# Performance work log

Measured on AMD Instinct MI355X. Metric: run time of the kernel, lower is better.

Reference implementation:

```python
import jax, jax.numpy as jnp
import numpy as np

B = 131072   # batched ODE states
D = 32       # state dim (net1 in/out)
H1 = 50      # net1 hidden
Q = 528      # tril(outer(y,y)) feature count = D*(D+1)//2
H2 = 700     # net2 hidden

# static lower-triangular index pairs for the quadratic feature expansion
_ROWS, _COLS = np.tril_indices(D)
_ROWS = jnp.asarray(_ROWS)
_COLS = jnp.asarray(_COLS)


def setup_inputs() -> dict:
    key = jax.random.key(0)
    ks = jax.random.split(key, 6)
    y = jax.random.normal(ks[0], (B, D), dtype=jnp.float32)
    t = jnp.zeros((1,), dtype=jnp.float32)  # unused by the dynamics
    # weights init: normal(0, 0.1), biases zero (as in the torch module)
    W1a = 0.1 * jax.random.normal(ks[1], (D, H1), dtype=jnp.float32)
    b1a = jnp.zeros((H1,), dtype=jnp.float32)
    W1b = 0.1 * jax.random.normal(ks[2], (H1, D), dtype=jnp.float32)
    b1b = jnp.zeros((D,), dtype=jnp.float32)
    W2a = 0.1 * jax.random.normal(ks[3], (Q, H2), dtype=jnp.float32)
    b2a = jnp.zeros((H2,), dtype=jnp.float32)
    W2b = 0.1 * jax.random.normal(ks[4], (H2, D), dtype=jnp.float32)
    b2b = jnp.zeros((D,), dtype=jnp.float32)
    return dict(t=t, y=y, W1a=W1a, b1a=b1a, W1b=W1b, b1b=b1b,
                W2a=W2a, b2a=b2a, W2b=W2b, b2b=b2b)


def reference(t, y, W1a, b1a, W1b, b1b, W2a, b2a, W2b, b2b):
    # quadratic_y: lower triangle of outer(y, y), vectorized over batch
    quad = y[:, _ROWS] * y[:, _COLS]               # [B, 528]
    out1 = jnp.tanh(y @ W1a + b1a) @ W1b + b1b     # [B, 32]
    out2 = jnp.tanh(quad @ W2a + b2a) @ W2b + b2b  # [B, 32]
    return out1 + out2
```

## Files before the change

kernel.cpp:

```cpp
#include <hip/hip_runtime.h>
#include <hip/hip_bf16.h>

#define B_TOT 131072
#define D     32
#define H1    50
#define QF    528
#define H2    700
#define MROWS 32
#define QSTR  584
#define KITER 18

typedef __attribute__((ext_vector_type(8))) short  short8x;
typedef __attribute__((ext_vector_type(4))) float  floatx4;

static __device__ __forceinline__ unsigned short f2bf(float f) {
    __hip_bfloat16 h = __float2bfloat16(f);
    return __builtin_bit_cast(unsigned short, h);
}
static __device__ __forceinline__ float bf2f(unsigned short u) {
    unsigned int x = (unsigned int)u << 16;
    return __builtin_bit_cast(float, x);
}
static __device__ __forceinline__ float tanh_fast(float x) {
    float e = __builtin_amdgcn_exp2f(x * 2.885390082f);
    return 1.f - 2.f * __builtin_amdgcn_rcpf(e + 1.f);
}

__global__ void prep_kernel(const float* __restrict__ W2a, const float* __restrict__ b2a,
                            const float* __restrict__ W2b,
                            const float* __restrict__ W1a, const float* __restrict__ b1a,
                            const float* __restrict__ W1b, const float* __restrict__ b1b,
                            const float* __restrict__ b2b,
                            unsigned short* __restrict__ W2aT,
                            unsigned short* __restrict__ W2bT) {
    int idx = blockIdx.x * 256 + threadIdx.x;
    const int N1 = KITER * 48 * 512;
    const int N2 = 16 * 4 * 512;
    if (idx < N1) {
        int k   = idx / (48 * 512);
        int rem = idx - k * (48 * 512);
        int p   = rem >> 9;
        int q   = rem & 511;
        int ln  = q >> 3, j = q & 7;
        int kk  = k * 32 + ((ln >> 4) << 3) + j;
        int c   = (p << 4) + (ln & 15);
        float v = 0.f;
        if (c < H2) {
            if (kk < QF)       v = W2a[kk * H2 + c];
            else if (kk == QF) v = b2a[c];
        } else if (c < H2 + H1) {
            int cc = c - H2;
            if (kk == QF)                        v = b1a[cc];
            else if (kk > QF && kk < QF + 1 + D) v = W1a[(kk - QF - 1) * H1 + cc];
        } else if (c == H2 + H1) {
            if (kk == QF) v = 1.0f;
        }
        W2aT[idx] = f2bf(v);
    } else if (idx < N1 + N2) {
        int i2 = idx - N1;
        int q  = i2 & 511;
        int ln = q >> 3, j = q & 7;
        int w  = i2 >> 11;
        int ks = (i2 >> 10) & 1;
        int of = (i2 >> 9) & 1;
        int kl = (ks << 5) + ((ln >> 4) << 3) + j;
        int kg = w * 48 + kl;
        int c  = (of << 4) + (ln & 15);
        float v = 0.f;
        if (kl < 48) {
            if (kg < H2)            v = W2b[kg * D + c];
            else if (kg < H2 + H1)  v = W1b[(kg - H2) * D + c];
            else if (kg == H2 + H1) v = (b1b[c] + b2b[c]) / tanh_fast(1.0f);
        }
        W2bT[i2] = f2bf(v);
    }
}

__global__ __launch_bounds__(1024, 8)
__attribute__((amdgpu_waves_per_eu(8, 8)))
void fused_kernel(
    const float* __restrict__ y,
    const unsigned short* __restrict__ W2aT, const unsigned short* __restrict__ W2bT,
    float* __restrict__ out) {

    __shared__ unsigned short quadls[MROWS][QSTR];
    __shared__ float          yls[MROWS][36];
    __shared__ unsigned short hst[16][16][68];

    const int tid  = threadIdx.x;
    const int lane = tid & 63;
    const int w    = tid >> 6;
    const int wu   = __builtin_amdgcn_readfirstlane(w);
    const int l15  = lane & 15;
    const int lg   = lane >> 4;
    const int row0 = blockIdx.x * MROWS;

    yls[tid >> 5][tid & 31] = y[row0 * D + tid];
    {
        int rr = lane >> 2, cc0 = 48 + (lane & 3) * 4;
        *reinterpret_cast<unsigned long long*>(&hst[w][rr][cc0]) = 0ULL;
    }
    __syncthreads();

    {
        int r = tid >> 5, i = tid & 31;
        int base = (i * (i + 1)) >> 1;
        float yi = yls[r][i];
        for (int j4 = 0; j4 <= i; j4 += 4) {
            floatx4 yv = *reinterpret_cast<const floatx4*>(&yls[r][j4]);
            #pragma unroll
            for (int jj = 0; jj < 4; ++jj) {
                int j = j4 + jj;
                if (j <= i) quadls[r][base + j] = f2bf(yi * yv[jj]);
            }
        }
        quadls[r][529 + i] = f2bf(yi);
        if (i == 0)  quadls[r][528] = (unsigned short)0x3F80;
        if (i < 15)  quadls[r][561 + i] = 0;
    }
    __syncthreads();

    floatx4 hacc00 = {0,0,0,0}, hacc01 = {0,0,0,0}, hacc02 = {0,0,0,0};
    floatx4 hacc10 = {0,0,0,0}, hacc11 = {0,0,0,0}, hacc12 = {0,0,0,0};
    {
        const unsigned short* bp = W2aT + wu * 3 * 512 + lane * 8;
        #pragma unroll 1
        for (int k = 0; k < KITER; ++k) {
            short8x a0 = *reinterpret_cast<const short8x*>(&quadls[l15][k * 32 + lg * 8]);
            short8x a1 = *reinterpret_cast<const short8x*>(&quadls[16 + l15][k * 32 + lg * 8]);
            short8x b0 = *reinterpret_cast<const short8x*>(bp);
            short8x b1 = *reinterpret_cast<const short8x*>(bp + 512);
            short8x b2 = *reinterpret_cast<const short8x*>(bp + 1024);
            hacc00 = __builtin_amdgcn_mfma_f32_16x16x32_bf16(a0, b0, hacc00, 0, 0, 0);
            hacc01 = __builtin_amdgcn_mfma_f32_16x16x32_bf16(a0, b1, hacc01, 0, 0, 0);
            hacc02 = __builtin_amdgcn_mfma_f32_16x16x32_bf16(a0, b2, hacc02, 0, 0, 0);
            hacc10 = __builtin_amdgcn_mfma_f32_16x16x32_bf16(a1, b0, hacc10, 0, 0, 0);
            hacc11 = __builtin_amdgcn_mfma_f32_16x16x32_bf16(a1, b1, hacc11, 0, 0, 0);
            hacc12 = __builtin_amdgcn_mfma_f32_16x16x32_bf16(a1, b2, hacc12, 0, 0, 0);
            bp += 48 * 512;
        }
    }
    __syncthreads();

    unsigned short* stage = &quadls[0][0];
    {
        const unsigned short* wb = W2bT + wu * 4 * 512 + lane * 8;
        #pragma unroll
        for (int m = 0; m < 2; ++m) {
            const floatx4 h0 = m ? hacc10 : hacc00;
            const floatx4 h1 = m ? hacc11 : hacc01;
            const floatx4 h2 = m ? hacc12 : hacc02;
            #pragma unroll
            for (int r = 0; r < 4; ++r) {
                hst[w][lg * 4 + r][l15]      = f2bf(tanh_fast(h0[r]));
                hst[w][lg * 4 + r][16 + l15] = f2bf(tanh_fast(h1[r]));
                hst[w][lg * 4 + r][32 + l15] = f2bf(tanh_fast(h2[r]));
            }
            short8x aa0 = *reinterpret_cast<const short8x*>(&hst[w][l15][lg * 8]);
            short8x aa1 = *reinterpret_cast<const short8x*>(&hst[w][l15][32 + lg * 8]);
            floatx4 o20 = {0,0,0,0}, o21 = {0,0,0,0};
            {
                short8x bw00 = *reinterpret_cast<const short8x*>(wb);
                short8x bw01 = *reinterpret_cast<const short8x*>(wb + 512);
                o20 = __builtin_amdgcn_mfma_f32_16x16x32_bf16(aa0, bw00, o20, 0, 0, 0);
                o21 = __builtin_amdgcn_mfma_f32_16x16x32_bf16(aa0, bw01, o21, 0, 0, 0);
            }
            {
                short8x bw10 = *reinterpret_cast<const short8x*>(wb + 1024);
                short8x bw11 = *reinterpret_cast<const short8x*>(wb + 1536);
                o20 = __builtin_amdgcn_mfma_f32_16x16x32_bf16(aa1, bw10, o20, 0, 0, 0);
                o21 = __builtin_amdgcn_mfma_f32_16x16x32_bf16(aa1, bw11, o21, 0, 0, 0);
            }
            #pragma unroll
            for (int r = 0; r < 4; ++r) {
                int row = m * 16 + lg * 4 + r;
                unsigned int pk = ((unsigned int)f2bf(o21[r]) << 16) | (unsigned int)f2bf(o20[r]);
                *reinterpret_cast<unsigned int*>(&stage[wu * 1024 + row * 32 + l15 * 2]) = pk;
            }
        }
    }
    __syncthreads();

    {
        int c  = tid & 31;
        int fr = (tid & ~31) + ((c & 15) << 1) + (c >> 4);
        float s0 = 0.f, s1 = 0.f;
        #pragma unroll
        for (int p = 0; p < 16; p += 2) {
            s0 += bf2f(stage[p * 1024 + fr]);
            s1 += bf2f(stage[(p + 1) * 1024 + fr]);
        }
        out[row0 * D + tid] = s0 + s1;
    }
}

extern "C" void kernel_launch(void* const* d_in, const int* in_sizes, int n_in,
                              void* d_out, int out_size, void* d_ws, size_t ws_size,
                              hipStream_t stream) {
    const float* y   = (const float*)d_in[1];
    const float* W1a = (const float*)d_in[2];
    const float* b1a = (const float*)d_in[3];
    const float* W1b = (const float*)d_in[4];
    const float* b1b = (const float*)d_in[5];
    const float* W2a = (const float*)d_in[6];
    const float* b2a = (const float*)d_in[7];
    const float* W2b = (const float*)d_in[8];
    const float* b2b = (const float*)d_in[9];

    unsigned short* W2aT = (unsigned short*)d_ws;
    unsigned short* W2bT = (unsigned short*)((char*)d_ws + 884736);

    const int prep_tasks = KITER * 48 * 512 + 16 * 4 * 512;
    prep_kernel<<<(prep_tasks + 255) / 256, 256, 0, stream>>>(
        W2a, b2a, W2b, W1a, b1a, W1b, b1b, b2b, W2aT, W2bT);
    fused_kernel<<<B_TOT / MROWS, 1024, 0, stream>>>(y, W2aT, W2bT, (float*)d_out);
}
```

Before: 164.4 us.

## Loop multiple row tiles per block and store quad features in MFMA fragment layout

Each block now processes 8 consecutive 32-row tiles in a loop, cutting the grid size by 8x. The quadratic features are scattered into LDS in the exact per-lane MFMA A-fragment order, so the GEMM loop reads contiguous 16-byte chunks per lane instead of strided rows. This aims to cut launch/tail overhead and LDS bank conflicts, at the cost of no overlap between tiles and scattered 2-byte LDS writes during feature construction.

```diff
diff --git a/kernel.cpp b/kernel.cpp
--- a/kernel.cpp
+++ b/kernel.cpp
@@ -7,8 +7,8 @@
 #define QF    528
 #define H2    700
 #define MROWS 32
-#define QSTR  584
 #define KITER 18
+#define TILES 8
 
 typedef __attribute__((ext_vector_type(8))) short  short8x;
 typedef __attribute__((ext_vector_type(4))) float  floatx4;
@@ -83,7 +83,7 @@
     const unsigned short* __restrict__ W2aT, const unsigned short* __restrict__ W2bT,
     float* __restrict__ out) {
 
-    __shared__ unsigned short quadls[MROWS][QSTR];
+    __shared__ unsigned short quadA[KITER][2][512];
     __shared__ float          yls[MROWS][36];
     __shared__ unsigned short hst[16][16][68];
 
@@ -93,104 +93,122 @@
     const int wu   = __builtin_amdgcn_readfirstlane(w);
     const int l15  = lane & 15;
     const int lg   = lane >> 4;
-    const int row0 = blockIdx.x * MROWS;
-
-    yls[tid >> 5][tid & 31] = y[row0 * D + tid];
+    unsigned short* stage = &quadA[0][0][0];
+
     {
         int rr = lane >> 2, cc0 = 48 + (lane & 3) * 4;
         *reinterpret_cast<unsigned long long*>(&hst[w][rr][cc0]) = 0ULL;
     }
-    __syncthreads();
-
-    {
-        int r = tid >> 5, i = tid & 31;
-        int base = (i * (i + 1)) >> 1;
-        float yi = yls[r][i];
-        for (int j4 = 0; j4 <= i; j4 += 4) {
-            floatx4 yv = *reinterpret_cast<const floatx4*>(&yls[r][j4]);
+
+    for (int t = 0; t < TILES; ++t) {
+        const int row0 = (blockIdx.x * TILES + t) * MROWS;
+
+        yls[tid >> 5][tid & 31] = y[row0 * D + tid];
+        __syncthreads();
+
+        {
+            int r = tid >> 5, i = tid & 31;
+            int rbase = ((r >> 4) << 9) + ((r & 15) << 3);
+            int base  = (i * (i + 1)) >> 1;
+            float yi  = yls[r][i];
+            for (int j4 = 0; j4 <= i; j4 += 4) {
+                floatx4 yv = *reinterpret_cast<const floatx4*>(&yls[r][j4]);
+                #pragma unroll
+                for (int jj = 0; jj < 4; ++jj) {
+                    int j = j4 + jj;
+                    if (j <= i) {
+                        int kk = base + j;
+                        stage[rbase + ((kk >> 5) << 10) + ((kk & 24) << 4) + (kk & 7)]
+                            = f2bf(yi * yv[jj]);
+                    }
+                }
+            }
+            {
+                int kk = 529 + i;
+                stage[rbase + ((kk >> 5) << 10) + ((kk & 24) << 4) + (kk & 7)] = f2bf(yi);
+            }
+            if (i == 0)
+                stage[rbase + ((528 >> 5) << 10) + ((528 & 24) << 4)] = (unsigned short)0x3F80;
+            if (i < 15) {
+                int kk = 561 + i;
+                stage[rbase + ((kk >> 5) << 10) + ((kk & 24) << 4) + (kk & 7)] = 0;
+            }
+        }
+        __syncthreads();
+
+        floatx4 hacc00 = {0,0,0,0}, hacc01 = {0,0,0,0}, hacc02 = {0,0,0,0};
+        floatx4 hacc10 = {0,0,0,0}, hacc11 = {0,0,0,0}, hacc12 = {0,0,0,0};
+        {
+            const unsigned short* bp = W2aT + wu * 3 * 512 + lane * 8;
+            const unsigned short* ap = &quadA[0][0][lane * 8];
+            #pragma unroll 1
+            for (int k = 0; k < KITER; ++k) {
+                short8x a0 = *reinterpret_cast<const short8x*>(ap);
+                short8x a1 = *reinterpret_cast<const short8x*>(ap + 512);
+                short8x b0 = *reinterpret_cast<const short8x*>(bp);
+                short8x b1 = *reinterpret_cast<const short8x*>(bp + 512);
+                short8x b2 = *reinterpret_cast<const short8x*>(bp + 1024);
+                hacc00 = __builtin_amdgcn_mfma_f32_16x16x32_bf16(a0, b0, hacc00, 0, 0, 0);
+                hacc01 = __builtin_amdgcn_mfma_f32_16x16x32_bf16(a0, b1, hacc01, 0, 0, 0);
+                hacc02 = __builtin_amdgcn_mfma_f32_16x16x32_bf16(a0, b2, hacc02, 0, 0, 0);
+                hacc10 = __builtin_amdgcn_mfma_f32_16x16x32_bf16(a1, b0, hacc10, 0, 0, 0);
+                hacc11 = __builtin_amdgcn_mfma_f32_16x16x32_bf16(a1, b1, hacc11, 0, 0, 0);
+                hacc12 = __builtin_amdgcn_mfma_f32_16x16x32_bf16(a1, b2, hacc12, 0, 0, 0);
+                ap += 1024;
+                bp += 48 * 512;
+            }
+        }
+        __syncthreads();
+
+        {
+            const unsigned short* wb = W2bT + wu * 4 * 512 + lane * 8;
             #pragma unroll
-            for (int jj = 0; jj < 4; ++jj) {
-                int j = j4 + jj;
-                if (j <= i) quadls[r][base + j] = f2bf(yi * yv[jj]);
-            }
-        }
-        quadls[r][529 + i] = f2bf(yi);
-        if (i == 0)  quadls[r][528] = (unsigned short)0x3F80;
-        if (i < 15)  quadls[r][561 + i] = 0;
-    }
-    __syncthreads();
-
-    floatx4 hacc00 = {0,0,0,0}, hacc01 = {0,0,0,0}, hacc02 = {0,0,0,0};
-    floatx4 hacc10 = {0,0,0,0}, hacc11 = {0,0,0,0}, hacc12 = {0,0,0,0};
-    {
-        const unsigned short* bp = W2aT + wu * 3 * 512 + lane * 8;
-        #pragma unroll 1
-        for (int k = 0; k < KITER; ++k) {
-            short8x a0 = *reinterpret_cast<const short8x*>(&quadls[l15][k * 32 + lg * 8]);
-            short8x a1 = *reinterpret_cast<const short8x*>(&quadls[16 + l15][k * 32 + lg * 8]);
-            short8x b0 = *reinterpret_cast<const short8x*>(bp);
-            short8x b1 = *reinterpret_cast<const short8x*>(bp + 512);
-            short8x b2 = *reinterpret_cast<const short8x*>(bp + 1024);
-            hacc00 = __builtin_amdgcn_mfma_f32_16x16x32_bf16(a0, b0, hacc00, 0, 0, 0);
-            hacc01 = __builtin_amdgcn_mfma_f32_16x16x32_bf16(a0, b1, hacc01, 0, 0, 0);
-            hacc02 = __builtin_amdgcn_mfma_f32_16x16x32_bf16(a0, b2, hacc02, 0, 0, 0);
-            hacc10 = __builtin_amdgcn_mfma_f32_16x16x32_bf16(a1, b0, hacc10, 0, 0, 0);
-            hacc11 = __builtin_amdgcn_mfma_f32_16x16x32_bf16(a1, b1, hacc11, 0, 0, 0);
-            hacc12 = __builtin_amdgcn_mfma_f32_16x16x32_bf16(a1, b2, hacc12, 0, 0, 0);
-            bp += 48 * 512;
-        }
-    }
-    __syncthreads();
-
-    unsigned short* stage = &quadls[0][0];
-    {
-        const unsigned short* wb = W2bT + wu * 4 * 512 + lane * 8;
-        #pragma unroll
-        for (int m = 0; m < 2; ++m) {
-            const floatx4 h0 = m ? hacc10 : hacc00;
-            const floatx4 h1 = m ? hacc11 : hacc01;
-            const floatx4 h2 = m ? hacc12 : hacc02;
+            for (int m = 0; m < 2; ++m) {
+                const floatx4 h0 = m ? hacc10 : hacc00;
+                const floatx4 h1 = m ? hacc11 : hacc01;
+                const floatx4 h2 = m ? hacc12 : hacc02;
+                #pragma unroll
+                for (int r = 0; r < 4; ++r) {
+                    hst[w][lg * 4 + r][l15]      = f2bf(tanh_fast(h0[r]));
+                    hst[w][lg * 4 + r][16 + l15] = f2bf(tanh_fast(h1[r]));
+                    hst[w][lg * 4 + r][32 + l15] = f2bf(tanh_fast(h2[r]));
+                }
+                short8x aa0 = *reinterpret_cast<const short8x*>(&hst[w][l15][lg * 8]);
+                short8x aa1 = *reinterpret_cast<const short8x*>(&hst[w][l15][32 + lg * 8]);
+                floatx4 o20 = {0,0,0,0}, o21 = {0,0,0,0};
+                {
+                    short8x bw00 = *reinterpret_cast<const short8x*>(wb);
+                    short8x bw01 = *reinterpret_cast<const short8x*>(wb + 512);
+                    o20 = __builtin_amdgcn_mfma_f32_16x16x32_bf16(aa0, bw00, o20, 0, 0, 0);
+                    o21 = __builtin_amdgcn_mfma_f32_16x16x32_bf16(aa0, bw01, o21, 0, 0, 0);
+                }
+                {
+                    short8x bw10 = *reinterpret_cast<const short8x*>(wb + 1024);
+                    short8x bw11 = *reinterpret_cast<const short8x*>(wb + 1536);
+                    o20 = __builtin_amdgcn_mfma_f32_16x16x32_bf16(aa1, bw10, o20, 0, 0, 0);
+                    o21 = __builtin_amdgcn_mfma_f32_16x16x32_bf16(aa1, bw11, o21, 0, 0, 0);
+                }
+                #pragma unroll
+                for (int r = 0; r < 4; ++r) {
+                    int row = m * 16 + lg * 4 + r;
+                    unsigned int pk = ((unsigned int)f2bf(o21[r]) << 16) | (unsigned int)f2bf(o20[r]);
+                    *reinterpret_cast<unsigned int*>(&stage[wu * 1024 + row * 32 + l15 * 2]) = pk;
+                }
+            }
+        }
+        __syncthreads();
+
+        {
+            int c  = tid & 31;
+            int fr = (tid & ~31) + ((c & 15) << 1) + (c >> 4);
+            float s0 = 0.f, s1 = 0.f;
             #pragma unroll
-            for (int r = 0; r < 4; ++r) {
-                hst[w][lg * 4 + r][l15]      = f2bf(tanh_fast(h0[r]));
-                hst[w][lg * 4 + r][16 + l15] = f2bf(tanh_fast(h1[r]));
-                hst[w][lg * 4 + r][32 + l15] = f2bf(tanh_fast(h2[r]));
-            }
-            short8x aa0 = *reinterpret_cast<const short8x*>(&hst[w][l15][lg * 8]);
-            short8x aa1 = *reinterpret_cast<const short8x*>(&hst[w][l15][32 + lg * 8]);
-            floatx4 o20 = {0,0,0,0}, o21 = {0,0,0,0};
-            {
-                short8x bw00 = *reinterpret_cast<const short8x*>(wb);
-                short8x bw01 = *reinterpret_cast<const short8x*>(wb + 512);
-                o20 = __builtin_amdgcn_mfma_f32_16x16x32_bf16(aa0, bw00, o20, 0, 0, 0);
-                o21 = __builtin_amdgcn_mfma_f32_16x16x32_bf16(aa0, bw01, o21, 0, 0, 0);
-            }
-            {
-                short8x bw10 = *reinterpret_cast<const short8x*>(wb + 1024);
-                short8x bw11 = *reinterpret_cast<const short8x*>(wb + 1536);
-                o20 = __builtin_amdgcn_mfma_f32_16x16x32_bf16(aa1, bw10, o20, 0, 0, 0);
-                o21 = __builtin_amdgcn_mfma_f32_16x16x32_bf16(aa1, bw11, o21, 0, 0, 0);
-            }
-            #pragma unroll
-            for (int r = 0; r < 4; ++r) {
-                int row = m * 16 + lg * 4 + r;
-                unsigned int pk = ((unsigned int)f2bf(o21[r]) << 16) | (unsigned int)f2bf(o20[r]);
-                *reinterpret_cast<unsigned int*>(&stage[wu * 1024 + row * 32 + l15 * 2]) = pk;
-            }
-        }
-    }
-    __syncthreads();
-
-    {
-        int c  = tid & 31;
-        int fr = (tid & ~31) + ((c & 15) << 1) + (c >> 4);
-        float s0 = 0.f, s1 = 0.f;
-        #pragma unroll
-        for (int p = 0; p < 16; p += 2) {
-            s0 += bf2f(stage[p * 1024 + fr]);
-            s1 += bf2f(stage[(p + 1) * 1024 + fr]);
-        }
-        out[row0 * D + tid] = s0 + s1;
+            for (int p = 0; p < 16; p += 2) {
+                s0 += bf2f(stage[p * 1024 + fr]);
+                s1 += bf2f(stage[(p + 1) * 1024 + fr]);
+            }
+            out[row0 * D + tid] = s0 + s1;
+        }
     }
 }
 
@@ -213,5 +231,5 @@
     const int prep_tasks = KITER * 48 * 512 + 16 * 4 * 512;
     prep_kernel<<<(prep_tasks + 255) / 256, 256, 0, stream>>>(
         W2a, b2a, W2b, W1a, b1a, W1b, b1b, b2b, W2aT, W2bT);
-    fused_kernel<<<B_TOT / MROWS, 1024, 0, stream>>>(y, W2aT, W2bT, (float*)d_out);
-}
+    fused_kernel<<<B_TOT / (MROWS * TILES), 1024, 0, stream>>>(y, W2aT, W2bT, (float*)d_out);
+}
```

Result: slower. 189.9 us (+15.5%).

## Process 64 rows per block to halve per-row weight fetches

Applied to the files above, without the earlier changes.

Each block now covers 64 batch rows instead of 32, so every wave runs four 16-row MFMA tiles against each set of W2a/W2b fragments it loads. This halves the global/L2 weight traffic per output row, which was large because every block streamed the full transposed weight matrix. In exchange the LDS footprint grows and the occupancy target drops from 8 to 4 waves per EU, with more accumulator registers per wave and less latency hiding.

```diff
diff --git a/kernel.cpp b/kernel.cpp
--- a/kernel.cpp
+++ b/kernel.cpp
@@ -6,7 +6,7 @@
 #define H1    50
 #define QF    528
 #define H2    700
-#define MROWS 32
+#define MROWS 64
 #define QSTR  584
 #define KITER 18
 
@@ -76,8 +76,8 @@
     }
 }
 
-__global__ __launch_bounds__(1024, 8)
-__attribute__((amdgpu_waves_per_eu(8, 8)))
+__global__ __launch_bounds__(1024)
+__attribute__((amdgpu_waves_per_eu(4, 4)))
 void fused_kernel(
     const float* __restrict__ y,
     const unsigned short* __restrict__ W2aT, const unsigned short* __restrict__ W2bT,
@@ -94,16 +94,20 @@
     const int l15  = lane & 15;
     const int lg   = lane >> 4;
     const int row0 = blockIdx.x * MROWS;
+    unsigned short* stage = &quadls[0][0];
 
     yls[tid >> 5][tid & 31] = y[row0 * D + tid];
+    yls[32 + (tid >> 5)][tid & 31] = y[row0 * D + 1024 + tid];
     {
         int rr = lane >> 2, cc0 = 48 + (lane & 3) * 4;
         *reinterpret_cast<unsigned long long*>(&hst[w][rr][cc0]) = 0ULL;
     }
     __syncthreads();
 
-    {
-        int r = tid >> 5, i = tid & 31;
+    #pragma unroll
+    for (int s = 0; s < 2; ++s) {
+        int task = tid + s * 1024;
+        int r = task >> 5, i = task & 31;
         int base = (i * (i + 1)) >> 1;
         float yi = yls[r][i];
         for (int j4 = 0; j4 <= i; j4 += 4) {
@@ -120,41 +124,42 @@
     }
     __syncthreads();
 
-    floatx4 hacc00 = {0,0,0,0}, hacc01 = {0,0,0,0}, hacc02 = {0,0,0,0};
-    floatx4 hacc10 = {0,0,0,0}, hacc11 = {0,0,0,0}, hacc12 = {0,0,0,0};
+    floatx4 hacc[4][3];
+    #pragma unroll
+    for (int m = 0; m < 4; ++m)
+        #pragma unroll
+        for (int nf = 0; nf < 3; ++nf) hacc[m][nf] = (floatx4){0.f, 0.f, 0.f, 0.f};
     {
         const unsigned short* bp = W2aT + wu * 3 * 512 + lane * 8;
-        #pragma unroll 1
+        #pragma unroll 2
         for (int k = 0; k < KITER; ++k) {
-            short8x a0 = *reinterpret_cast<const short8x*>(&quadls[l15][k * 32 + lg * 8]);
-            short8x a1 = *reinterpret_cast<const short8x*>(&quadls[16 + l15][k * 32 + lg * 8]);
+            short8x a[4];
+            #pragma unroll
+            for (int m = 0; m < 4; ++m)
+                a[m] = *reinterpret_cast<const short8x*>(&quadls[m * 16 + l15][k * 32 + lg * 8]);
             short8x b0 = *reinterpret_cast<const short8x*>(bp);
             short8x b1 = *reinterpret_cast<const short8x*>(bp + 512);
             short8x b2 = *reinterpret_cast<const short8x*>(bp + 1024);
-            hacc00 = __builtin_amdgcn_mfma_f32_16x16x32_bf16(a0, b0, hacc00, 0, 0, 0);
-            hacc01 = __builtin_amdgcn_mfma_f32_16x16x32_bf16(a0, b1, hacc01, 0, 0, 0);
-            hacc02 = __builtin_amdgcn_mfma_f32_16x16x32_bf16(a0, b2, hacc02, 0, 0, 0);
-            hacc10 = __builtin_amdgcn_mfma_f32_16x16x32_bf16(a1, b0, hacc10, 0, 0, 0);
-            hacc11 = __builtin_amdgcn_mfma_f32_16x16x32_bf16(a1, b1, hacc11, 0, 0, 0);
-            hacc12 = __builtin_amdgcn_mfma_f32_16x16x32_bf16(a1, b2, hacc12, 0, 0, 0);
+            #pragma unroll
+            for (int m = 0; m < 4; ++m) {
+                hacc[m][0] = __builtin_amdgcn_mfma_f32_16x16x32_bf16(a[m], b0, hacc[m][0], 0, 0, 0);
+                hacc[m][1] = __builtin_amdgcn_mfma_f32_16x16x32_bf16(a[m], b1, hacc[m][1], 0, 0, 0);
+                hacc[m][2] = __builtin_amdgcn_mfma_f32_16x16x32_bf16(a[m], b2, hacc[m][2], 0, 0, 0);
+            }
             bp += 48 * 512;
         }
     }
     __syncthreads();
 
-    unsigned short* stage = &quadls[0][0];
     {
         const unsigned short* wb = W2bT + wu * 4 * 512 + lane * 8;
         #pragma unroll
-        for (int m = 0; m < 2; ++m) {
-            const floatx4 h0 = m ? hacc10 : hacc00;
-            const floatx4 h1 = m ? hacc11 : hacc01;
-            const floatx4 h2 = m ? hacc12 : hacc02;
+        for (int m = 0; m < 4; ++m) {
             #pragma unroll
             for (int r = 0; r < 4; ++r) {
-                hst[w][lg * 4 + r][l15]      = f2bf(tanh_fast(h0[r]));
-                hst[w][lg * 4 + r][16 + l15] = f2bf(tanh_fast(h1[r]));
-                hst[w][lg * 4 + r][32 + l15] = f2bf(tanh_fast(h2[r]));
+                hst[w][lg * 4 + r][l15]      = f2bf(tanh_fast(hacc[m][0][r]));
+                hst[w][lg * 4 + r][16 + l15] = f2bf(tanh_fast(hacc[m][1][r]));
+                hst[w][lg * 4 + r][32 + l15] = f2bf(tanh_fast(hacc[m][2][r]));
             }
             short8x aa0 = *reinterpret_cast<const short8x*>(&hst[w][l15][lg * 8]);
             short8x aa1 = *reinterpret_cast<const short8x*>(&hst[w][l15][32 + lg * 8]);
@@ -175,22 +180,26 @@
             for (int r = 0; r < 4; ++r) {
                 int row = m * 16 + lg * 4 + r;
                 unsigned int pk = ((unsigned int)f2bf(o21[r]) << 16) | (unsigned int)f2bf(o20[r]);
-                *reinterpret_cast<unsigned int*>(&stage[wu * 1024 + row * 32 + l15 * 2]) = pk;
-            }
-        }
-    }
-    __syncthreads();
-
-    {
-        int c  = tid & 31;
-        int fr = (tid & ~31) + ((c & 15) << 1) + (c >> 4);
-        float s0 = 0.f, s1 = 0.f;
+                *reinterpret_cast<unsigned int*>(&stage[wu * 2048 + row * 32 + l15 * 2]) = pk;
+            }
+        }
+    }
+    __syncthreads();
+
+    {
         #pragma unroll
-        for (int p = 0; p < 16; p += 2) {
-            s0 += bf2f(stage[p * 1024 + fr]);
-            s1 += bf2f(stage[(p + 1) * 1024 + fr]);
-        }
-        out[row0 * D + tid] = s0 + s1;
+        for (int s = 0; s < 2; ++s) {
+            int e  = tid + s * 1024;
+            int c  = e & 31;
+            int fr = (e & ~31) + ((c & 15) << 1) + (c >> 4);
+            float s0 = 0.f, s1 = 0.f;
+            #pragma unroll
+            for (int p = 0; p < 16; p += 2) {
+                s0 += bf2f(stage[p * 2048 + fr]);
+                s1 += bf2f(stage[(p + 1) * 2048 + fr]);
+            }
+            out[row0 * D + e] = s0 + s1;
+        }
     }
 }
 
```

New measurement: 152.1 us. 7.5% less time.
